# Kernel optimization log

Measured on AMD Instinct MI355X. Metric: run time of the kernel, lower is better.

Reference implementation:

```python
import jax, jax.numpy as jnp
import numpy as np

B, R, N, F = 8, 8, 1024, 256


def setup_inputs() -> dict:
    key = jax.random.key(0)
    k1, k2 = jax.random.split(key)
    inputs = jax.random.normal(k1, (B, R, N, F), dtype=jnp.float32)
    Bs = jax.random.normal(k2, (R, F, F), dtype=jnp.float32) * 0.05
    return {"inputs": inputs, "Bs": Bs}


def reference(inputs, Bs):
    # E_r @ B_r : [B,R,N,F] x [R,F,F] -> [B,R,N,F]
    e = jnp.einsum("brnf,rfg->brng", inputs, Bs)
    # (E_r B_r) @ E_r^T : [B,R,N,F] x [B,R,M,F] -> [B,R,N,M]
    scores = jnp.einsum("brng,brmg->brnm", e, inputs)
    return jax.nn.sigmoid(scores)
```

## Files before the change

kernel.cpp:

```cpp
#include <hip/hip_runtime.h>


typedef float    f32x4 __attribute__((ext_vector_type(4)));
typedef _Float16 f16x8 __attribute__((ext_vector_type(8)));
typedef _Float16 f16x4 __attribute__((ext_vector_type(4)));

#define WS_E_OFF   0
#define WS_BST_OFF 16777216

__global__ __launch_bounds__(256) void bl_convert(
    const float* __restrict__ E, const float* __restrict__ Bs,
    _Float16* __restrict__ wsE, _Float16* __restrict__ wsBsT) {
  int bid = blockIdx.x, tid = threadIdx.x;
  if (bid < 8192) {
    int cid = (bid << 8) + tid;
    int br  = cid >> 15;
    int rem = cid & 32767;
    int fc  = rem >> 10;
    int n   = rem & 1023;
    const float* src = E + ((size_t)br << 18) + n * 256 + (fc << 3);
    f32x4 v0 = *(const f32x4*)src;
    f32x4 v1 = *(const f32x4*)(src + 4);
    f16x8 h;
    h[0] = (_Float16)v0[0]; h[1] = (_Float16)v0[1];
    h[2] = (_Float16)v0[2]; h[3] = (_Float16)v0[3];
    h[4] = (_Float16)v1[0]; h[5] = (_Float16)v1[1];
    h[6] = (_Float16)v1[2]; h[7] = (_Float16)v1[3];
    *(f16x8*)(wsE + ((size_t)br << 18) + (fc << 13) + (n << 3)) = h;
  } else {
    int cid = ((bid - 8192) << 8) + tid;
    int r   = cid >> 13;
    int rem = cid & 8191;
    int fc  = rem >> 8;
    int g   = rem & 255;
    const float* src = Bs + (r << 16) + (fc << 3) * 256 + g;
    f16x8 h;
#pragma unroll
    for (int j = 0; j < 8; ++j) h[j] = (_Float16)src[j * 256];
    *(f16x8*)(wsBsT + (r << 16) + (fc << 11) + (g << 3)) = h;
  }
}

__global__ __launch_bounds__(512, 2) void bl_fused(
    const _Float16* __restrict__ wsE, const _Float16* __restrict__ wsBsT,
    float* __restrict__ out) {
  __shared__ _Float16 se[32768];
  __shared__ _Float16 stg[32768];
  int b0  = blockIdx.x;
  int bid = ((b0 & 7) << 6) + (b0 >> 3);
  int br  = bid >> 3;
  int nb  = bid & 7;
  int n0  = nb << 7;
  int r   = br & 7;
  int tid = threadIdx.x;
  int lane = tid & 63, wave = tid >> 6;
  int quad = lane >> 4, l16 = lane & 15;
  int wg  = wave >> 1;
  int wnn = wave & 1;

  const _Float16* eG  = wsE + ((size_t)br << 18);
  const _Float16* bsG = wsBsT + (r << 16);

  f32x4 acc[4][4] = {};

  for (int kk = 0; kk < 4; ++kk) {
    f16x8 va[2], vb[4];
#pragma unroll
    for (int i = 0; i < 2; ++i) {
      int c = (i << 9) + tid;
      int kcl = c >> 7, nl = c & 127;
      va[i] = *(const f16x8*)(eG + (((kk << 3) + kcl) << 13) + ((n0 + nl) << 3));
    }
#pragma unroll
    for (int i = 0; i < 4; ++i) {
      int c = (i << 9) + tid;
      int kcl = c >> 8, gl = c & 255;
      vb[i] = *(const f16x8*)(bsG + (((kk << 3) + kcl) << 11) + (gl << 3));
    }
    __syncthreads();
#pragma unroll
    for (int i = 0; i < 2; ++i) {
      int c = (i << 9) + tid;
      *(f16x8*)&stg[c << 3] = va[i];
    }
#pragma unroll
    for (int i = 0; i < 4; ++i) {
      int c = (i << 9) + tid;
      *(f16x8*)&stg[8192 + (c << 3)] = vb[i];
    }
    __syncthreads();
#pragma unroll
    for (int ks = 0; ks < 2; ++ks) {
      int kc = (ks << 2) + quad;
      f16x8 af[4], bf[4];
#pragma unroll
      for (int rt = 0; rt < 4; ++rt)
        af[rt] = *(const f16x8*)&stg[((kc << 7) + (wnn << 6) + (rt << 4) + l16) << 3];
#pragma unroll
      for (int ct = 0; ct < 4; ++ct)
        bf[ct] = *(const f16x8*)&stg[8192 + (((kc << 8) + (wg << 6) + (ct << 4) + l16) << 3)];
#pragma unroll
      for (int rt = 0; rt < 4; ++rt)
#pragma unroll
        for (int ct = 0; ct < 4; ++ct)
          acc[rt][ct] = __builtin_amdgcn_mfma_f32_16x16x32_f16(bf[ct], af[rt], acc[rt][ct], 0, 0, 0);
    }
  }
#pragma unroll
  for (int rt = 0; rt < 4; ++rt) {
    int n = (wnn << 6) + (rt << 4) + l16;
#pragma unroll
    for (int ct = 0; ct < 4; ++ct) {
      int g  = (wg << 6) + (ct << 4) + (quad << 2);
      int gc = g >> 3, gj = g & 7;
      f16x4 h;
#pragma unroll
      for (int i = 0; i < 4; ++i) h[i] = (_Float16)acc[rt][ct][i];
      *(f16x4*)&se[(gc << 10) + (n << 3) + gj] = h;
    }
  }

  f16x8 vs[4];
#pragma unroll
  for (int i = 0; i < 4; ++i) {
    int c = (i << 9) + tid;
    int kcl = c >> 8, ml = c & 255;
    vs[i] = *(const f16x8*)(eG + (kcl << 13) + (ml << 3));
  }
#pragma unroll
  for (int rt = 0; rt < 4; ++rt)
#pragma unroll
    for (int ct = 0; ct < 4; ++ct) acc[rt][ct] = (f32x4){0.f, 0.f, 0.f, 0.f};
  __syncthreads();

  float* oB = out + ((size_t)br << 20);
  int buf = 0;
  for (int jj = 0; jj < 16; ++jj) {
    int kk = jj & 3;
#pragma unroll
    for (int i = 0; i < 4; ++i) {
      int c = (i << 9) + tid;
      *(f16x8*)&stg[(buf << 14) + (c << 3)] = vs[i];
    }
    __syncthreads();
    if (jj < 15) {
      int j2 = jj + 1;
      int mt2 = j2 >> 2, kk2 = j2 & 3;
#pragma unroll
      for (int i = 0; i < 4; ++i) {
        int c = (i << 9) + tid;
        int kcl = c >> 8, ml = c & 255;
        vs[i] = *(const f16x8*)(eG + (((kk2 << 3) + kcl) << 13) + (((mt2 << 8) + ml) << 3));
      }
    }
#pragma unroll
    for (int ks = 0; ks < 2; ++ks) {
      int kc = (ks << 2) + quad;
      f16x8 af[4], bf[4];
#pragma unroll
      for (int rt = 0; rt < 4; ++rt)
        af[rt] = *(const f16x8*)&se[((((kk << 3) + kc) << 7) + (wnn << 6) + (rt << 4) + l16) << 3];
#pragma unroll
      for (int ct = 0; ct < 4; ++ct)
        bf[ct] = *(const f16x8*)&stg[(buf << 14) + (((kc << 8) + (wg << 6) + (ct << 4) + l16) << 3)];
#pragma unroll
      for (int rt = 0; rt < 4; ++rt)
#pragma unroll
        for (int ct = 0; ct < 4; ++ct)
          acc[rt][ct] = __builtin_amdgcn_mfma_f32_16x16x32_f16(bf[ct], af[rt], acc[rt][ct], 0, 0, 0);
    }
    if (kk == 3) {
      int mt = jj >> 2;
#pragma unroll
      for (int rt = 0; rt < 4; ++rt) {
        int n = n0 + (wnn << 6) + (rt << 4) + l16;
#pragma unroll
        for (int ct = 0; ct < 4; ++ct) {
          int m = (mt << 8) + (wg << 6) + (ct << 4) + (quad << 2);
          f32x4 v;
#pragma unroll
          for (int i = 0; i < 4; ++i) {
            float x = acc[rt][ct][i];
            v[i] = __builtin_amdgcn_rcpf(1.0f + __expf(-x));
          }
          *(f32x4*)(oB + ((size_t)n << 10) + m) = v;
          acc[rt][ct] = (f32x4){0.f, 0.f, 0.f, 0.f};
        }
      }
    }
    buf ^= 1;
  }
}

extern "C" void kernel_launch(void* const* d_in, const int* in_sizes, int n_in,
                              void* d_out, int out_size, void* d_ws, size_t ws_size,
                              hipStream_t stream) {
  const float* E  = (const float*)d_in[0];
  const float* Bs = (const float*)d_in[1];
  _Float16* wsE   = (_Float16*)d_ws + WS_E_OFF;
  _Float16* wsBsT = (_Float16*)d_ws + WS_BST_OFF;
  float* out = (float*)d_out;

  bl_convert<<<8448, 256, 0, stream>>>(E, Bs, wsE, wsBsT);
  bl_fused<<<512, 512, 0, stream>>>(wsE, wsBsT, out);
}
```

Before: 378.4 us.

## Load second-GEMM E tiles straight into registers, dropping LDS staging and barriers

The second GEMM phase no longer stages E^T tiles through shared memory with a barrier each iteration. Each wave now loads its B operand fragments straight from global memory into double-buffered registers and computes a larger 128x64 output tile per wave with 8x4 accumulators. The M tile grows to 512, so there are two output passes. This removes LDS store/load traffic and 16 block barriers and shrinks the shared staging buffer. The cost is much higher register pressure (128 accumulator VGPRs plus 16 fragment registers), which risks spills or lower occupancy, and global loads are now uncoalesced per-wave fragment loads.

```diff
diff --git a/kernel.cpp b/kernel.cpp
--- a/kernel.cpp
+++ b/kernel.cpp
@@ -45,7 +45,7 @@
     const _Float16* __restrict__ wsE, const _Float16* __restrict__ wsBsT,
     float* __restrict__ out) {
   __shared__ _Float16 se[32768];
-  __shared__ _Float16 stg[32768];
+  __shared__ _Float16 stg[24576];
   int b0  = blockIdx.x;
   int bid = ((b0 & 7) << 6) + (b0 >> 3);
   int br  = bid >> 3;
@@ -55,140 +55,123 @@
   int tid = threadIdx.x;
   int lane = tid & 63, wave = tid >> 6;
   int quad = lane >> 4, l16 = lane & 15;
-  int wg  = wave >> 1;
-  int wnn = wave & 1;
 
   const _Float16* eG  = wsE + ((size_t)br << 18);
   const _Float16* bsG = wsBsT + (r << 16);
 
-  f32x4 acc[4][4] = {};
-
-  for (int kk = 0; kk < 4; ++kk) {
-    f16x8 va[2], vb[4];
+  {
+    int wg  = wave >> 1;
+    int wnn = wave & 1;
+    f32x4 acc[4][4] = {};
+    for (int kk = 0; kk < 4; ++kk) {
+      f16x8 va[2], vb[4];
 #pragma unroll
-    for (int i = 0; i < 2; ++i) {
-      int c = (i << 9) + tid;
-      int kcl = c >> 7, nl = c & 127;
-      va[i] = *(const f16x8*)(eG + (((kk << 3) + kcl) << 13) + ((n0 + nl) << 3));
+      for (int i = 0; i < 2; ++i) {
+        int c = (i << 9) + tid;
+        int kcl = c >> 7, nl = c & 127;
+        va[i] = *(const f16x8*)(eG + (((kk << 3) + kcl) << 13) + ((n0 + nl) << 3));
+      }
+#pragma unroll
+      for (int i = 0; i < 4; ++i) {
+        int c = (i << 9) + tid;
+        int kcl = c >> 8, gl = c & 255;
+        vb[i] = *(const f16x8*)(bsG + (((kk << 3) + kcl) << 11) + (gl << 3));
+      }
+      __syncthreads();
+#pragma unroll
+      for (int i = 0; i < 2; ++i) {
+        int c = (i << 9) + tid;
+        *(f16x8*)&stg[c << 3] = va[i];
+      }
+#pragma unroll
+      for (int i = 0; i < 4; ++i) {
+        int c = (i << 9) + tid;
+        *(f16x8*)&stg[8192 + (c << 3)] = vb[i];
+      }
+      __syncthreads();
+#pragma unroll
+      for (int ks = 0; ks < 2; ++ks) {
+        int kc = (ks << 2) + quad;
+        f16x8 af[4], bf[4];
+#pragma unroll
+        for (int rt = 0; rt < 4; ++rt)
+          af[rt] = *(const f16x8*)&stg[((kc << 7) + (wnn << 6) + (rt << 4) + l16) << 3];
+#pragma unroll
+        for (int ct = 0; ct < 4; ++ct)
+          bf[ct] = *(const f16x8*)&stg[8192 + (((kc << 8) + (wg << 6) + (ct << 4) + l16) << 3)];
+#pragma unroll
+        for (int rt = 0; rt < 4; ++rt)
+#pragma unroll
+          for (int ct = 0; ct < 4; ++ct)
+            acc[rt][ct] = __builtin_amdgcn_mfma_f32_16x16x32_f16(bf[ct], af[rt], acc[rt][ct], 0, 0, 0);
+      }
     }
 #pragma unroll
-    for (int i = 0; i < 4; ++i) {
-      int c = (i << 9) + tid;
-      int kcl = c >> 8, gl = c & 255;
-      vb[i] = *(const f16x8*)(bsG + (((kk << 3) + kcl) << 11) + (gl << 3));
-    }
-    __syncthreads();
+    for (int rt = 0; rt < 4; ++rt) {
+      int n = (wnn << 6) + (rt << 4) + l16;
 #pragma unroll
-    for (int i = 0; i < 2; ++i) {
-      int c = (i << 9) + tid;
-      *(f16x8*)&stg[c << 3] = va[i];
-    }
+      for (int ct = 0; ct < 4; ++ct) {
+        int g  = (wg << 6) + (ct << 4) + (quad << 2);
+        int gc = g >> 3, gj = g & 7;
+        f16x4 h;
 #pragma unroll
-    for (int i = 0; i < 4; ++i) {
-      int c = (i << 9) + tid;
-      *(f16x8*)&stg[8192 + (c << 3)] = vb[i];
-    }
-    __syncthreads();
-#pragma unroll
-    for (int ks = 0; ks < 2; ++ks) {
-      int kc = (ks << 2) + quad;
-      f16x8 af[4], bf[4];
-#pragma unroll
-      for (int rt = 0; rt < 4; ++rt)
-        af[rt] = *(const f16x8*)&stg[((kc << 7) + (wnn << 6) + (rt << 4) + l16) << 3];
-#pragma unroll
-      for (int ct = 0; ct < 4; ++ct)
-        bf[ct] = *(const f16x8*)&stg[8192 + (((kc << 8) + (wg << 6) + (ct << 4) + l16) << 3)];
-#pragma unroll
-      for (int rt = 0; rt < 4; ++rt)
-#pragma unroll
-        for (int ct = 0; ct < 4; ++ct)
-          acc[rt][ct] = __builtin_amdgcn_mfma_f32_16x16x32_f16(bf[ct], af[rt], acc[rt][ct], 0, 0, 0);
-    }
-  }
-#pragma unroll
-  for (int rt = 0; rt < 4; ++rt) {
-    int n = (wnn << 6) + (rt << 4) + l16;
-#pragma unroll
-    for (int ct = 0; ct < 4; ++ct) {
-      int g  = (wg << 6) + (ct << 4) + (quad << 2);
-      int gc = g >> 3, gj = g & 7;
-      f16x4 h;
-#pragma unroll
-      for (int i = 0; i < 4; ++i) h[i] = (_Float16)acc[rt][ct][i];
-      *(f16x4*)&se[(gc << 10) + (n << 3) + gj] = h;
+        for (int i = 0; i < 4; ++i) h[i] = (_Float16)acc[rt][ct][i];
+        *(f16x4*)&se[(gc << 10) + (n << 3) + gj] = h;
+      }
     }
   }
 
-  f16x8 vs[4];
+  int mw0 = (wave >> 1) << 7;
+  int nn  = (wave & 1) << 6;
+
+  f32x4 acc2[8][4] = {};
+  f16x8 bf[2][8];
+
 #pragma unroll
-  for (int i = 0; i < 4; ++i) {
-    int c = (i << 9) + tid;
-    int kcl = c >> 8, ml = c & 255;
-    vs[i] = *(const f16x8*)(eG + (kcl << 13) + (ml << 3));
-  }
-#pragma unroll
-  for (int rt = 0; rt < 4; ++rt)
-#pragma unroll
-    for (int ct = 0; ct < 4; ++ct) acc[rt][ct] = (f32x4){0.f, 0.f, 0.f, 0.f};
+  for (int mf = 0; mf < 8; ++mf)
+    bf[0][mf] = *(const f16x8*)(eG + (quad << 13) + ((mw0 + (mf << 4) + l16) << 3));
+
   __syncthreads();
 
   float* oB = out + ((size_t)br << 20);
-  int buf = 0;
-  for (int jj = 0; jj < 16; ++jj) {
-    int kk = jj & 3;
 #pragma unroll
-    for (int i = 0; i < 4; ++i) {
-      int c = (i << 9) + tid;
-      *(f16x8*)&stg[(buf << 14) + (c << 3)] = vs[i];
+  for (int g = 0; g < 16; ++g) {
+    const int p  = g & 1;
+    const int mt = g >> 3;
+    if (g < 15) {
+      const int g2   = g + 1;
+      const int kcb2 = (((g2 >> 1) & 3) << 3) + ((g2 & 1) << 2);
+      const int mb2  = ((g2 >> 3) << 9) + mw0;
+#pragma unroll
+      for (int mf = 0; mf < 8; ++mf)
+        bf[p ^ 1][mf] = *(const f16x8*)(eG + ((kcb2 + quad) << 13) + ((mb2 + (mf << 4) + l16) << 3));
     }
-    __syncthreads();
-    if (jj < 15) {
-      int j2 = jj + 1;
-      int mt2 = j2 >> 2, kk2 = j2 & 3;
+    const int kcq = (((g >> 1) & 3) << 3) + ((g & 1) << 2) + quad;
+    f16x8 af[4];
 #pragma unroll
-      for (int i = 0; i < 4; ++i) {
-        int c = (i << 9) + tid;
-        int kcl = c >> 8, ml = c & 255;
-        vs[i] = *(const f16x8*)(eG + (((kk2 << 3) + kcl) << 13) + (((mt2 << 8) + ml) << 3));
-      }
-    }
+    for (int rt = 0; rt < 4; ++rt)
+      af[rt] = *(const f16x8*)&se[((kcq << 7) + nn + (rt << 4) + l16) << 3];
 #pragma unroll
-    for (int ks = 0; ks < 2; ++ks) {
-      int kc = (ks << 2) + quad;
-      f16x8 af[4], bf[4];
+    for (int mf = 0; mf < 8; ++mf)
 #pragma unroll
       for (int rt = 0; rt < 4; ++rt)
-        af[rt] = *(const f16x8*)&se[((((kk << 3) + kc) << 7) + (wnn << 6) + (rt << 4) + l16) << 3];
+        acc2[mf][rt] = __builtin_amdgcn_mfma_f32_16x16x32_f16(bf[p][mf], af[rt], acc2[mf][rt], 0, 0, 0);
+    if (g == 7 || g == 15) {
+      const int mb = (mt << 9) + mw0 + (quad << 2);
 #pragma unroll
-      for (int ct = 0; ct < 4; ++ct)
-        bf[ct] = *(const f16x8*)&stg[(buf << 14) + (((kc << 8) + (wg << 6) + (ct << 4) + l16) << 3)];
+      for (int mf = 0; mf < 8; ++mf) {
 #pragma unroll
-      for (int rt = 0; rt < 4; ++rt)
-#pragma unroll
-        for (int ct = 0; ct < 4; ++ct)
-          acc[rt][ct] = __builtin_amdgcn_mfma_f32_16x16x32_f16(bf[ct], af[rt], acc[rt][ct], 0, 0, 0);
-    }
-    if (kk == 3) {
-      int mt = jj >> 2;
-#pragma unroll
-      for (int rt = 0; rt < 4; ++rt) {
-        int n = n0 + (wnn << 6) + (rt << 4) + l16;
-#pragma unroll
-        for (int ct = 0; ct < 4; ++ct) {
-          int m = (mt << 8) + (wg << 6) + (ct << 4) + (quad << 2);
+        for (int rt = 0; rt < 4; ++rt) {
+          int n = n0 + nn + (rt << 4) + l16;
           f32x4 v;
 #pragma unroll
-          for (int i = 0; i < 4; ++i) {
-            float x = acc[rt][ct][i];
-            v[i] = __builtin_amdgcn_rcpf(1.0f + __expf(-x));
-          }
-          *(f32x4*)(oB + ((size_t)n << 10) + m) = v;
-          acc[rt][ct] = (f32x4){0.f, 0.f, 0.f, 0.f};
+          for (int i = 0; i < 4; ++i)
+            v[i] = __builtin_amdgcn_rcpf(1.0f + __expf(-acc2[mf][rt][i]));
+          *(f32x4*)(oB + ((size_t)n << 10) + mb + (mf << 4)) = v;
+          acc2[mf][rt] = (f32x4){0.f, 0.f, 0.f, 0.f};
         }
       }
     }
-    buf ^= 1;
   }
 }
 
```

New measurement: 393.4 us. 1.04x slower.
